# Optimization experiments

Hardware: AMD Instinct MI355X
Metric: run time of the kernel (lower is better)

## Reference

```python
import jax, jax.numpy as jnp
import numpy as np

N = 524288          # batch size
NUM_SD = 64         # socio-demographic chars
H = 128             # hidden size of TasteParams MLP
NUM_ALT_FEAT = 9    # alternative features
NUM_CLASSES = 3
# utility_structure: class k -> (start, end) column slice of x
SEGMENTS = [(0, 3), (3, 6), (6, 9)]


def setup_inputs() -> dict:
    key = jax.random.key(0)
    ks = jax.random.split(key, 8)
    s = 0.05
    return {
        "x": jax.random.normal(ks[0], (N, NUM_ALT_FEAT), jnp.float32),
        "z": jax.random.normal(ks[1], (N, NUM_SD), jnp.float32),
        "W1": jax.random.normal(ks[2], (NUM_SD, H), jnp.float32) * s,
        "b1": jax.random.normal(ks[3], (H,), jnp.float32) * s,
        "W2": jax.random.normal(ks[4], (H, H), jnp.float32) * s,
        "b2": jax.random.normal(ks[5], (H,), jnp.float32) * s,
        "W3": jax.random.normal(ks[6], (H, NUM_ALT_FEAT + NUM_CLASSES), jnp.float32) * s,
        "b3": jax.random.normal(ks[7], (NUM_ALT_FEAT + NUM_CLASSES,), jnp.float32) * s,
    }


def _forward(x, z, W1, b1, W2, b2, W3, b3):
    # TasteParams MLP: Linear-ReLU-Linear-ReLU-Linear
    h = jax.nn.relu(z @ W1 + b1)
    h = jax.nn.relu(h @ W2 + b2)
    b = h @ W3 + b3                        # (N, 12)
    # monotonic_constraints (num_classes==3, func_intercept=True)
    b = jnp.concatenate([
        -jax.nn.relu(-b[:, :6]),
        b[:, 6:7],
        -jax.nn.relu(-b[:, 7:9]),
        b[:, -NUM_CLASSES:],
    ], axis=1)
    taste = b[:, :NUM_ALT_FEAT]            # (N, 9)
    intercept = b[:, -NUM_CLASSES:]        # (N, 3)
    # MNL_layer with b: per-segment elementwise mult + reduce into logits column
    prod = x * taste                       # (N, 9)
    logits = jnp.stack(
        [prod[:, lo:hi].sum(axis=1) for (lo, hi) in SEGMENTS], axis=1
    )                                      # (N, 3)
    return logits + intercept


def reference(x, z, W1, b1, W2, b2, W3, b3):
    return _forward(x, z, W1, b1, W2, b2, W3, b3)
```

## Files before the change

### kernel.cpp

```cpp
#include <hip/hip_runtime.h>
#include <hip/hip_bf16.h>


typedef __bf16 bf16x8 __attribute__((ext_vector_type(8)));
typedef float  f32x16 __attribute__((ext_vector_type(16)));
typedef unsigned int uint2v __attribute__((ext_vector_type(2)));
typedef unsigned int uint4v __attribute__((ext_vector_type(4)));

#define MFMA32(a, b, c) __builtin_amdgcn_mfma_f32_32x32x16_bf16((a), (b), (c), 0, 0, 0)
#define PIN_AGPR(v) asm("" : "+a"(v))

#define SW3 0
#define SW1 1536
#define SW2 9728
#define SB1 26112
#define SB2 26240
#define SB3 26368
#define SMEM_ELTS 26384

#define NBLK    512
#define NTILE   16384
#define WSTRIDE (NBLK * 4)

__device__ __forceinline__ unsigned pkbf(float lo, float hi) {
  unsigned short lb = __builtin_bit_cast(unsigned short, (__bf16)lo);
  unsigned short hb = __builtin_bit_cast(unsigned short, (__bf16)hi);
  return ((unsigned)hb << 16) | (unsigned)lb;
}

template <int SUB>
__device__ __forceinline__ bf16x8 mk_bfrag(const f32x16 h) {
  constexpr int B = SUB * 8;
  unsigned p01 = pkbf(h[B + 0], h[B + 1]);
  unsigned p23 = pkbf(h[B + 2], h[B + 3]);
  unsigned p45 = pkbf(h[B + 4], h[B + 5]);
  unsigned p67 = pkbf(h[B + 6], h[B + 7]);
  unsigned d0, d1, d2, d3;
#if __has_builtin(__builtin_amdgcn_permlane32_swap)
  uint2v r1 = __builtin_amdgcn_permlane32_swap(p01, p45, false, false);
  uint2v r2 = __builtin_amdgcn_permlane32_swap(p23, p67, false, false);
  d0 = r1[0]; d2 = r1[1];
  d1 = r2[0]; d3 = r2[1];
#else
  int hi = (threadIdx.x >> 5) & 1;
  unsigned sp01 = (unsigned)__shfl_xor((int)p01, 32, 64);
  unsigned sp23 = (unsigned)__shfl_xor((int)p23, 32, 64);
  unsigned sp45 = (unsigned)__shfl_xor((int)p45, 32, 64);
  unsigned sp67 = (unsigned)__shfl_xor((int)p67, 32, 64);
  d0 = hi ? sp45 : p01;
  d2 = hi ? p45  : sp01;
  d1 = hi ? sp67 : p23;
  d3 = hi ? p67  : sp23;
#endif
  uint4v t; t[0] = d0; t[1] = d1; t[2] = d2; t[3] = d3;
  return __builtin_bit_cast(bf16x8, t);
}

__device__ __forceinline__ bf16x8 ldw(const __bf16* sm, int vaddr, int imm) {
  return *(const bf16x8*)((const char*)sm + vaddr + imm);
}

__device__ __forceinline__ bf16x8 biasA(__bf16 v) {
  bf16x8 f;
  #pragma unroll
  for (int i = 0; i < 8; ++i) f[i] = (__bf16)0.0f;
  f[0] = v;
  return f;
}

__global__ __launch_bounds__(256, 2)
void tastenet_kernel(const float* __restrict__ x, const float* __restrict__ z,
                     const float* __restrict__ W1, const float* __restrict__ b1,
                     const float* __restrict__ W2, const float* __restrict__ b2,
                     const float* __restrict__ W3, const float* __restrict__ b3,
                     float* __restrict__ out) {
  __shared__ __align__(16) __bf16 sm[SMEM_ELTS];
  const int tid = threadIdx.x;
  unsigned* smw = (unsigned*)sm;

  for (int i = tid; i < 4096; i += 256) {
    int m = i & 127, k = (i >> 7) * 2;
    smw[SW1 / 2 + m * 32 + (((k >> 3) ^ (m & 7)) << 2) + ((k >> 1) & 3)] =
        pkbf(W1[k * 128 + m], W1[(k + 1) * 128 + m]);
  }
  for (int i = tid; i < 8192; i += 256) {
    int m = i & 127, k = (i >> 7) * 2;
    smw[SW2 / 2 + m * 64 + (((k >> 3) ^ (m & 7)) << 2) + ((k >> 1) & 3)] =
        pkbf(W2[k * 128 + m], W2[(k + 1) * 128 + m]);
  }
  for (int i = tid; i < 768; i += 256) {
    int kk = i / 12, m = i - kk * 12, k = kk * 2;
    smw[SW3 / 2 + m * 64 + (((k >> 3) ^ (m & 7)) << 2) + ((k >> 1) & 3)] =
        pkbf(W3[k * 12 + m], W3[(k + 1) * 12 + m]);
  }
  if (tid < 128) { sm[SB1 + tid] = (__bf16)b1[tid]; sm[SB2 + tid] = (__bf16)b2[tid]; }
  if (tid < 12)  sm[SB3 + tid] = (__bf16)b3[tid];
  __syncthreads();

  const int wave = tid >> 6;
  const int lane = tid & 63;
  const int q    = lane >> 5;
  const int n    = lane & 31;
  const int s8   = n & 7;
  const int eq   = q ^ (s8 & 1);
  const int sh   = s8 >> 1;

  int aw1[4], aw2[4];
  #pragma unroll
  for (int j = 0; j < 4; ++j) {
    aw1[j] = n * 128 + eq * 16 + 32 * (j ^ sh);
    aw2[j] = n * 256 + eq * 16 + 32 * (j ^ sh);
  }

  bf16x8 ones;
  #pragma unroll
  for (int i = 0; i < 8; ++i) ones[i] = (__bf16)0.0f;
  if (q == 0) ones[0] = (__bf16)1.0f;
  PIN_AGPR(ones);

  bf16x8 ba1[4], ba2[4], ba3;
  #pragma unroll
  for (int f = 0; f < 4; ++f) {
    ba1[f] = biasA((q == 0) ? sm[SB1 + f * 32 + n] : (__bf16)0.0f);
    ba2[f] = biasA((q == 0) ? sm[SB2 + f * 32 + n] : (__bf16)0.0f);
    PIN_AGPR(ba1[f]); PIN_AGPR(ba2[f]);
  }
  ba3 = biasA((q == 0 && n < 12) ? sm[SB3 + n] : (__bf16)0.0f);
  PIN_AGPR(ba3);

  f32x16 zeroC;
  #pragma unroll
  for (int i = 0; i < 16; ++i) zeroC[i] = 0.0f;
  PIN_AGPR(zeroC);

  const int wid = blockIdx.x * 4 + wave;

  float4 zv[8];
  {
    const float* zr = z + ((long)wid * 32 + n) * 64;
    #pragma unroll
    for (int kt = 0; kt < 4; ++kt) {
      zv[2 * kt]     = *(const float4*)(zr + kt * 16 + q * 8);
      zv[2 * kt + 1] = *(const float4*)(zr + kt * 16 + q * 8 + 4);
    }
  }

  #pragma unroll 1
  for (int t = wid; t < NTILE; t += WSTRIDE) {
    const long row = (long)t * 32 + n;

    const float* xr = x + row * 9;
    float xv0 = xr[q * 4 + 0], xv1 = xr[q * 4 + 1];
    float xv2 = xr[q * 4 + 2], xv3 = xr[q * 4 + 3];
    float xv4 = xr[8];

    bf16x8 bz[4];
    #pragma unroll
    for (int kt = 0; kt < 4; ++kt) {
      float4 a = zv[2 * kt], b = zv[2 * kt + 1];
      bf16x8 f;
      f[0] = (__bf16)a.x; f[1] = (__bf16)a.y; f[2] = (__bf16)a.z; f[3] = (__bf16)a.w;
      f[4] = (__bf16)b.x; f[5] = (__bf16)b.y; f[6] = (__bf16)b.z; f[7] = (__bf16)b.w;
      bz[kt] = f;
    }

    if (t + WSTRIDE < NTILE) {
      const float* zr = z + ((long)(t + WSTRIDE) * 32 + n) * 64;
      #pragma unroll
      for (int kt = 0; kt < 4; ++kt) {
        zv[2 * kt]     = *(const float4*)(zr + kt * 16 + q * 8);
        zv[2 * kt + 1] = *(const float4*)(zr + kt * 16 + q * 8 + 4);
      }
    }

    bf16x8 bf2[8];
    #pragma unroll
    for (int fp = 0; fp < 2; ++fp) {
      f32x16 aA = MFMA32(ba1[2 * fp + 0], ones, zeroC);
      f32x16 aB = MFMA32(ba1[2 * fp + 1], ones, zeroC);
      PIN_AGPR(aA); PIN_AGPR(aB);
      #pragma unroll
      for (int kt = 0; kt < 4; ++kt) {
        aA = MFMA32(ldw(sm, aw1[kt], SW1 * 2 + (2 * fp + 0) * 4096), bz[kt], aA);
        aB = MFMA32(ldw(sm, aw1[kt], SW1 * 2 + (2 * fp + 1) * 4096), bz[kt], aB);
      }
      #pragma unroll
      for (int i = 0; i < 16; ++i) { aA[i] = fmaxf(aA[i], 0.0f); aB[i] = fmaxf(aB[i], 0.0f); }
      bf2[4 * fp + 0] = mk_bfrag<0>(aA);
      bf2[4 * fp + 1] = mk_bfrag<1>(aA);
      bf2[4 * fp + 2] = mk_bfrag<0>(aB);
      bf2[4 * fp + 3] = mk_bfrag<1>(aB);
    }

    f32x16 acc3 = MFMA32(ba3, ones, zeroC);
    PIN_AGPR(acc3);
    #pragma unroll
    for (int fp = 0; fp < 2; ++fp) {
      f32x16 aA = MFMA32(ba2[2 * fp + 0], ones, zeroC);
      f32x16 aB = MFMA32(ba2[2 * fp + 1], ones, zeroC);
      PIN_AGPR(aA); PIN_AGPR(aB);
      #pragma unroll
      for (int kt = 0; kt < 8; ++kt) {
        aA = MFMA32(ldw(sm, aw2[kt & 3], SW2 * 2 + (2 * fp + 0) * 8192 + 128 * (kt >> 2)),
                    bf2[kt], aA);
        aB = MFMA32(ldw(sm, aw2[kt & 3], SW2 * 2 + (2 * fp + 1) * 8192 + 128 * (kt >> 2)),
                    bf2[kt], aB);
      }
      #pragma unroll
      for (int i = 0; i < 16; ++i) { aA[i] = fmaxf(aA[i], 0.0f); aB[i] = fmaxf(aB[i], 0.0f); }
      acc3 = MFMA32(ldw(sm, aw2[0], SW3 * 2 + 128 * fp), mk_bfrag<0>(aA), acc3);
      acc3 = MFMA32(ldw(sm, aw2[1], SW3 * 2 + 128 * fp), mk_bfrag<1>(aA), acc3);
      acc3 = MFMA32(ldw(sm, aw2[2], SW3 * 2 + 128 * fp), mk_bfrag<0>(aB), acc3);
      acc3 = MFMA32(ldw(sm, aw2[3], SW3 * 2 + 128 * fp), mk_bfrag<1>(aB), acc3);
    }

    float t0 = acc3[0], t1 = acc3[1], t2 = acc3[2], t3 = acc3[3];
    float t4 = acc3[4], t5 = acc3[5], t6 = acc3[6], t7 = acc3[7];
    float o0 = 0.f, o1 = 0.f, o2 = 0.f, g1v = 0.f, g2v = 0.f;
    if (q == 0) {
      t0 = fminf(t0, 0.0f); t1 = fminf(t1, 0.0f);
      t2 = fminf(t2, 0.0f); t3 = fminf(t3, 0.0f);
      t4 = fminf(t4, 0.0f);
      o0 = xv0 * t0 + xv1 * t1 + xv2 * t2 + t5;
      o1 = xv3 * t3 + t6;
      o2 = xv4 * t4 + t7;
    } else {
      t0 = fminf(t0, 0.0f); t1 = fminf(t1, 0.0f);
      t3 = fminf(t3, 0.0f);
      g1v = xv0 * t0 + xv1 * t1;
      g2v = xv2 * t2 + xv3 * t3;
    }
    float a1v = __shfl_xor(g1v, 32, 64);
    float a2v = __shfl_xor(g2v, 32, 64);
    if (q == 0) {
      float* op = out + row * 3;
      op[0] = o0;
      op[1] = o1 + a1v;
      op[2] = o2 + a2v;
    }
  }
}

extern "C" void kernel_launch(void* const* d_in, const int* in_sizes, int n_in,
                              void* d_out, int out_size, void* d_ws, size_t ws_size,
                              hipStream_t stream) {
  const float* x  = (const float*)d_in[0];
  const float* z  = (const float*)d_in[1];
  const float* W1 = (const float*)d_in[2];
  const float* b1 = (const float*)d_in[3];
  const float* W2 = (const float*)d_in[4];
  const float* b2 = (const float*)d_in[5];
  const float* W3 = (const float*)d_in[6];
  const float* b3 = (const float*)d_in[7];
  tastenet_kernel<<<dim3(NBLK), dim3(256), 0, stream>>>(
      x, z, W1, b1, W2, b2, W3, b3, (float*)d_out);
}
```

Before: 234.7 us.

## Reload bias fragments from LDS per tile and raise occupancy to three blocks

Stops keeping the nine bias A-fragments pinned in AGPRs for the whole kernel. Each tile now reloads them from LDS, using an opaque zero offset so the compiler cannot hoist the loads back out of the loop. The z-to-bf16 conversion for the next tile moves to the middle of the current tile, behind a sched_barrier. The freed registers let launch_bounds ask for 3 blocks per CU, and the grid grows to 768 blocks to match; the cost is extra LDS reads and VALU work on every tile.

After: 281.9 us. +20.1%, slower.

```diff
diff --git a/kernel.cpp b/kernel.cpp
--- a/kernel.cpp
+++ b/kernel.cpp
@@ -18,7 +18,7 @@
 #define SB3 26368
 #define SMEM_ELTS 26384
 
-#define NBLK    512
+#define NBLK    768
 #define NTILE   16384
 #define WSTRIDE (NBLK * 4)
 
@@ -68,7 +68,7 @@
   return f;
 }
 
-__global__ __launch_bounds__(256, 2)
+__global__ __launch_bounds__(256, 3)
 void tastenet_kernel(const float* __restrict__ x, const float* __restrict__ z,
                      const float* __restrict__ W1, const float* __restrict__ b1,
                      const float* __restrict__ W2, const float* __restrict__ b2,
@@ -118,16 +118,6 @@
   if (q == 0) ones[0] = (__bf16)1.0f;
   PIN_AGPR(ones);
 
-  bf16x8 ba1[4], ba2[4], ba3;
-  #pragma unroll
-  for (int f = 0; f < 4; ++f) {
-    ba1[f] = biasA((q == 0) ? sm[SB1 + f * 32 + n] : (__bf16)0.0f);
-    ba2[f] = biasA((q == 0) ? sm[SB2 + f * 32 + n] : (__bf16)0.0f);
-    PIN_AGPR(ba1[f]); PIN_AGPR(ba2[f]);
-  }
-  ba3 = biasA((q == 0 && n < 12) ? sm[SB3 + n] : (__bf16)0.0f);
-  PIN_AGPR(ba3);
-
   f32x16 zeroC;
   #pragma unroll
   for (int i = 0; i < 16; ++i) zeroC[i] = 0.0f;
@@ -136,6 +126,7 @@
   const int wid = blockIdx.x * 4 + wave;
 
   float4 zv[8];
+  bf16x8 bz[4];
   {
     const float* zr = z + ((long)wid * 32 + n) * 64;
     #pragma unroll
@@ -143,18 +134,6 @@
       zv[2 * kt]     = *(const float4*)(zr + kt * 16 + q * 8);
       zv[2 * kt + 1] = *(const float4*)(zr + kt * 16 + q * 8 + 4);
     }
-  }
-
-  #pragma unroll 1
-  for (int t = wid; t < NTILE; t += WSTRIDE) {
-    const long row = (long)t * 32 + n;
-
-    const float* xr = x + row * 9;
-    float xv0 = xr[q * 4 + 0], xv1 = xr[q * 4 + 1];
-    float xv2 = xr[q * 4 + 2], xv3 = xr[q * 4 + 3];
-    float xv4 = xr[8];
-
-    bf16x8 bz[4];
     #pragma unroll
     for (int kt = 0; kt < 4; ++kt) {
       float4 a = zv[2 * kt], b = zv[2 * kt + 1];
@@ -163,6 +142,19 @@
       f[4] = (__bf16)b.x; f[5] = (__bf16)b.y; f[6] = (__bf16)b.z; f[7] = (__bf16)b.w;
       bz[kt] = f;
     }
+  }
+
+  #pragma unroll 1
+  for (int t = wid; t < NTILE; t += WSTRIDE) {
+    const long row = (long)t * 32 + n;
+
+    int zt;
+    asm volatile("v_mov_b32 %0, 0" : "=v"(zt));
+
+    const float* xr = x + row * 9;
+    float xv0 = xr[q * 4 + 0], xv1 = xr[q * 4 + 1];
+    float xv2 = xr[q * 4 + 2], xv3 = xr[q * 4 + 3];
+    float xv4 = xr[8];
 
     if (t + WSTRIDE < NTILE) {
       const float* zr = z + ((long)(t + WSTRIDE) * 32 + n) * 64;
@@ -176,8 +168,12 @@
     bf16x8 bf2[8];
     #pragma unroll
     for (int fp = 0; fp < 2; ++fp) {
-      f32x16 aA = MFMA32(ba1[2 * fp + 0], ones, zeroC);
-      f32x16 aB = MFMA32(ba1[2 * fp + 1], ones, zeroC);
+      f32x16 aA = MFMA32(
+          biasA((q == 0) ? sm[SB1 + zt + (2 * fp + 0) * 32 + n] : (__bf16)0.0f),
+          ones, zeroC);
+      f32x16 aB = MFMA32(
+          biasA((q == 0) ? sm[SB1 + zt + (2 * fp + 1) * 32 + n] : (__bf16)0.0f),
+          ones, zeroC);
       PIN_AGPR(aA); PIN_AGPR(aB);
       #pragma unroll
       for (int kt = 0; kt < 4; ++kt) {
@@ -192,12 +188,29 @@
       bf2[4 * fp + 3] = mk_bfrag<1>(aB);
     }
 
-    f32x16 acc3 = MFMA32(ba3, ones, zeroC);
+    if (t + WSTRIDE < NTILE) {
+      #pragma unroll
+      for (int kt = 0; kt < 4; ++kt) {
+        float4 a = zv[2 * kt], b = zv[2 * kt + 1];
+        bf16x8 f;
+        f[0] = (__bf16)a.x; f[1] = (__bf16)a.y; f[2] = (__bf16)a.z; f[3] = (__bf16)a.w;
+        f[4] = (__bf16)b.x; f[5] = (__bf16)b.y; f[6] = (__bf16)b.z; f[7] = (__bf16)b.w;
+        bz[kt] = f;
+      }
+    }
+    __builtin_amdgcn_sched_barrier(0);
+
+    f32x16 acc3 = MFMA32(
+        biasA((q == 0 && n < 12) ? sm[SB3 + zt + n] : (__bf16)0.0f), ones, zeroC);
     PIN_AGPR(acc3);
     #pragma unroll
     for (int fp = 0; fp < 2; ++fp) {
-      f32x16 aA = MFMA32(ba2[2 * fp + 0], ones, zeroC);
-      f32x16 aB = MFMA32(ba2[2 * fp + 1], ones, zeroC);
+      f32x16 aA = MFMA32(
+          biasA((q == 0) ? sm[SB2 + zt + (2 * fp + 0) * 32 + n] : (__bf16)0.0f),
+          ones, zeroC);
+      f32x16 aB = MFMA32(
+          biasA((q == 0) ? sm[SB2 + zt + (2 * fp + 1) * 32 + n] : (__bf16)0.0f),
+          ones, zeroC);
       PIN_AGPR(aA); PIN_AGPR(aB);
       #pragma unroll
       for (int kt = 0; kt < 8; ++kt) {
```

## Widen MFMA chains to four accumulators and split layer-3 reduction

Applied to the files above, without the earlier changes.

Layers 1 and 2 now keep four independent 32x32 accumulators live at once instead of processing two at a time, which gives the MFMA pipeline more independent work and hides dependency latency. The bf16 conversion of the next tile's z is moved into the loop body after layer 1, behind a scheduling barrier. The layer-3 reduction is split into two accumulator chains that are summed at the end to shorten the serial dependency. In exchange, more AGPR/VGPR pressure could hurt the occupancy of two blocks per CU or cause spills.

Measured after the change: 247.6 us. 1.06x slower.

```diff
diff --git a/kernel.cpp b/kernel.cpp
--- a/kernel.cpp
+++ b/kernel.cpp
@@ -136,6 +136,7 @@
   const int wid = blockIdx.x * 4 + wave;
 
   float4 zv[8];
+  bf16x8 bz[4];
   {
     const float* zr = z + ((long)wid * 32 + n) * 64;
     #pragma unroll
@@ -143,18 +144,6 @@
       zv[2 * kt]     = *(const float4*)(zr + kt * 16 + q * 8);
       zv[2 * kt + 1] = *(const float4*)(zr + kt * 16 + q * 8 + 4);
     }
-  }
-
-  #pragma unroll 1
-  for (int t = wid; t < NTILE; t += WSTRIDE) {
-    const long row = (long)t * 32 + n;
-
-    const float* xr = x + row * 9;
-    float xv0 = xr[q * 4 + 0], xv1 = xr[q * 4 + 1];
-    float xv2 = xr[q * 4 + 2], xv3 = xr[q * 4 + 3];
-    float xv4 = xr[8];
-
-    bf16x8 bz[4];
     #pragma unroll
     for (int kt = 0; kt < 4; ++kt) {
       float4 a = zv[2 * kt], b = zv[2 * kt + 1];
@@ -163,6 +152,16 @@
       f[4] = (__bf16)b.x; f[5] = (__bf16)b.y; f[6] = (__bf16)b.z; f[7] = (__bf16)b.w;
       bz[kt] = f;
     }
+  }
+
+  #pragma unroll 1
+  for (int t = wid; t < NTILE; t += WSTRIDE) {
+    const long row = (long)t * 32 + n;
+
+    const float* xr = x + row * 9;
+    float xv0 = xr[q * 4 + 0], xv1 = xr[q * 4 + 1];
+    float xv2 = xr[q * 4 + 2], xv3 = xr[q * 4 + 3];
+    float xv4 = xr[8];
 
     if (t + WSTRIDE < NTILE) {
       const float* zr = z + ((long)(t + WSTRIDE) * 32 + n) * 64;
@@ -173,49 +172,76 @@
       }
     }
 
+    f32x16 d0 = MFMA32(ba1[0], ones, zeroC);
+    f32x16 d1 = MFMA32(ba1[1], ones, zeroC);
+    f32x16 d2 = MFMA32(ba1[2], ones, zeroC);
+    f32x16 d3 = MFMA32(ba1[3], ones, zeroC);
+    PIN_AGPR(d0); PIN_AGPR(d1); PIN_AGPR(d2); PIN_AGPR(d3);
+    #pragma unroll
+    for (int kt = 0; kt < 4; ++kt) {
+      d0 = MFMA32(ldw(sm, aw1[kt], SW1 * 2 + 0 * 4096), bz[kt], d0);
+      d1 = MFMA32(ldw(sm, aw1[kt], SW1 * 2 + 1 * 4096), bz[kt], d1);
+      d2 = MFMA32(ldw(sm, aw1[kt], SW1 * 2 + 2 * 4096), bz[kt], d2);
+      d3 = MFMA32(ldw(sm, aw1[kt], SW1 * 2 + 3 * 4096), bz[kt], d3);
+    }
+    #pragma unroll
+    for (int i = 0; i < 16; ++i) {
+      d0[i] = fmaxf(d0[i], 0.0f); d1[i] = fmaxf(d1[i], 0.0f);
+      d2[i] = fmaxf(d2[i], 0.0f); d3[i] = fmaxf(d3[i], 0.0f);
+    }
     bf16x8 bf2[8];
-    #pragma unroll
-    for (int fp = 0; fp < 2; ++fp) {
-      f32x16 aA = MFMA32(ba1[2 * fp + 0], ones, zeroC);
-      f32x16 aB = MFMA32(ba1[2 * fp + 1], ones, zeroC);
-      PIN_AGPR(aA); PIN_AGPR(aB);
+    bf2[0] = mk_bfrag<0>(d0); bf2[1] = mk_bfrag<1>(d0);
+    bf2[2] = mk_bfrag<0>(d1); bf2[3] = mk_bfrag<1>(d1);
+    bf2[4] = mk_bfrag<0>(d2); bf2[5] = mk_bfrag<1>(d2);
+    bf2[6] = mk_bfrag<0>(d3); bf2[7] = mk_bfrag<1>(d3);
+
+    if (t + WSTRIDE < NTILE) {
       #pragma unroll
       for (int kt = 0; kt < 4; ++kt) {
-        aA = MFMA32(ldw(sm, aw1[kt], SW1 * 2 + (2 * fp + 0) * 4096), bz[kt], aA);
-        aB = MFMA32(ldw(sm, aw1[kt], SW1 * 2 + (2 * fp + 1) * 4096), bz[kt], aB);
+        float4 a = zv[2 * kt], b = zv[2 * kt + 1];
+        bf16x8 f;
+        f[0] = (__bf16)a.x; f[1] = (__bf16)a.y; f[2] = (__bf16)a.z; f[3] = (__bf16)a.w;
+        f[4] = (__bf16)b.x; f[5] = (__bf16)b.y; f[6] = (__bf16)b.z; f[7] = (__bf16)b.w;
+        bz[kt] = f;
       }
-      #pragma unroll
-      for (int i = 0; i < 16; ++i) { aA[i] = fmaxf(aA[i], 0.0f); aB[i] = fmaxf(aB[i], 0.0f); }
-      bf2[4 * fp + 0] = mk_bfrag<0>(aA);
-      bf2[4 * fp + 1] = mk_bfrag<1>(aA);
-      bf2[4 * fp + 2] = mk_bfrag<0>(aB);
-      bf2[4 * fp + 3] = mk_bfrag<1>(aB);
-    }
-
-    f32x16 acc3 = MFMA32(ba3, ones, zeroC);
-    PIN_AGPR(acc3);
-    #pragma unroll
-    for (int fp = 0; fp < 2; ++fp) {
-      f32x16 aA = MFMA32(ba2[2 * fp + 0], ones, zeroC);
-      f32x16 aB = MFMA32(ba2[2 * fp + 1], ones, zeroC);
-      PIN_AGPR(aA); PIN_AGPR(aB);
-      #pragma unroll
-      for (int kt = 0; kt < 8; ++kt) {
-        aA = MFMA32(ldw(sm, aw2[kt & 3], SW2 * 2 + (2 * fp + 0) * 8192 + 128 * (kt >> 2)),
-                    bf2[kt], aA);
-        aB = MFMA32(ldw(sm, aw2[kt & 3], SW2 * 2 + (2 * fp + 1) * 8192 + 128 * (kt >> 2)),
-                    bf2[kt], aB);
-      }
-      #pragma unroll
-      for (int i = 0; i < 16; ++i) { aA[i] = fmaxf(aA[i], 0.0f); aB[i] = fmaxf(aB[i], 0.0f); }
-      acc3 = MFMA32(ldw(sm, aw2[0], SW3 * 2 + 128 * fp), mk_bfrag<0>(aA), acc3);
-      acc3 = MFMA32(ldw(sm, aw2[1], SW3 * 2 + 128 * fp), mk_bfrag<1>(aA), acc3);
-      acc3 = MFMA32(ldw(sm, aw2[2], SW3 * 2 + 128 * fp), mk_bfrag<0>(aB), acc3);
-      acc3 = MFMA32(ldw(sm, aw2[3], SW3 * 2 + 128 * fp), mk_bfrag<1>(aB), acc3);
-    }
-
-    float t0 = acc3[0], t1 = acc3[1], t2 = acc3[2], t3 = acc3[3];
-    float t4 = acc3[4], t5 = acc3[5], t6 = acc3[6], t7 = acc3[7];
+    }
+    __builtin_amdgcn_sched_barrier(0);
+
+    f32x16 c0 = MFMA32(ba2[0], ones, zeroC);
+    f32x16 c1 = MFMA32(ba2[1], ones, zeroC);
+    f32x16 c2 = MFMA32(ba2[2], ones, zeroC);
+    f32x16 c3 = MFMA32(ba2[3], ones, zeroC);
+    PIN_AGPR(c0); PIN_AGPR(c1); PIN_AGPR(c2); PIN_AGPR(c3);
+    #pragma unroll
+    for (int kt = 0; kt < 8; ++kt) {
+      const int ro = 128 * (kt >> 2);
+      c0 = MFMA32(ldw(sm, aw2[kt & 3], SW2 * 2 + 0 * 8192 + ro), bf2[kt], c0);
+      c1 = MFMA32(ldw(sm, aw2[kt & 3], SW2 * 2 + 1 * 8192 + ro), bf2[kt], c1);
+      c2 = MFMA32(ldw(sm, aw2[kt & 3], SW2 * 2 + 2 * 8192 + ro), bf2[kt], c2);
+      c3 = MFMA32(ldw(sm, aw2[kt & 3], SW2 * 2 + 3 * 8192 + ro), bf2[kt], c3);
+    }
+    #pragma unroll
+    for (int i = 0; i < 16; ++i) {
+      c0[i] = fmaxf(c0[i], 0.0f); c1[i] = fmaxf(c1[i], 0.0f);
+      c2[i] = fmaxf(c2[i], 0.0f); c3[i] = fmaxf(c3[i], 0.0f);
+    }
+
+    f32x16 a3a = MFMA32(ba3, ones, zeroC);
+    PIN_AGPR(a3a);
+    a3a = MFMA32(ldw(sm, aw2[0], SW3 * 2 + 0),   mk_bfrag<0>(c0), a3a);
+    f32x16 a3b = MFMA32(ldw(sm, aw2[0], SW3 * 2 + 128), mk_bfrag<0>(c2), zeroC);
+    PIN_AGPR(a3b);
+    a3a = MFMA32(ldw(sm, aw2[1], SW3 * 2 + 0),   mk_bfrag<1>(c0), a3a);
+    a3b = MFMA32(ldw(sm, aw2[1], SW3 * 2 + 128), mk_bfrag<1>(c2), a3b);
+    a3a = MFMA32(ldw(sm, aw2[2], SW3 * 2 + 0),   mk_bfrag<0>(c1), a3a);
+    a3b = MFMA32(ldw(sm, aw2[2], SW3 * 2 + 128), mk_bfrag<0>(c3), a3b);
+    a3a = MFMA32(ldw(sm, aw2[3], SW3 * 2 + 0),   mk_bfrag<1>(c1), a3a);
+    a3b = MFMA32(ldw(sm, aw2[3], SW3 * 2 + 128), mk_bfrag<1>(c3), a3b);
+
+    float t0 = a3a[0] + a3b[0], t1 = a3a[1] + a3b[1];
+    float t2 = a3a[2] + a3b[2], t3 = a3a[3] + a3b[3];
+    float t4 = a3a[4] + a3b[4], t5 = a3a[5] + a3b[5];
+    float t6 = a3a[6] + a3b[6], t7 = a3a[7] + a3b[7];
     float o0 = 0.f, o1 = 0.f, o2 = 0.f, g1v = 0.f, g2v = 0.f;
     if (q == 0) {
       t0 = fminf(t0, 0.0f); t1 = fminf(t1, 0.0f);
```

## Prefetch z tiles directly into swizzled LDS with global_load_lds

Applied to the files above, without the earlier changes.

Replaces the register-held float4 prefetch of the next z tile with asynchronous global-to-LDS DMA loads into a per-wave, XOR-swizzled LDS slot. Each tile's z fragments are then read back from LDS and converted to bf16. The block grows to 8 waves (512 threads) over 256 blocks, and LDS use rises accordingly. The goal is to free the registers that held in-flight z data and to keep global loads asynchronous. The cost is more LDS traffic, a full vmcnt wait at every iteration, and the large LDS footprint limiting residency to one block per CU.

Measured after the change: 241.1 us. 1.03x slower.

```diff
diff --git a/kernel.cpp b/kernel.cpp
--- a/kernel.cpp
+++ b/kernel.cpp
@@ -16,11 +16,20 @@
 #define SB1 26112
 #define SB2 26240
 #define SB3 26368
-#define SMEM_ELTS 26384
-
-#define NBLK    512
+#define ZS_BYTE 52768
+#define SMEM_ELTS (26384 + 32768)
+
+#define NBLK    256
+#define NTHR    512
 #define NTILE   16384
-#define WSTRIDE (NBLK * 4)
+#define WSTRIDE (NBLK * 8)
+
+typedef __attribute__((address_space(3))) unsigned int lds_u32;
+typedef __attribute__((address_space(1))) const unsigned int glb_u32;
+
+__device__ __forceinline__ void gll16(const float* g, const void* l) {
+  __builtin_amdgcn_global_load_lds((glb_u32*)g, (lds_u32*)l, 16, 0, 0);
+}
 
 __device__ __forceinline__ unsigned pkbf(float lo, float hi) {
   unsigned short lb = __builtin_bit_cast(unsigned short, (__bf16)lo);
@@ -60,6 +69,10 @@
   return *(const bf16x8*)((const char*)sm + vaddr + imm);
 }
 
+__device__ __forceinline__ float4 ldz(const __bf16* sm, int vaddr) {
+  return *(const float4*)((const char*)sm + vaddr);
+}
+
 __device__ __forceinline__ bf16x8 biasA(__bf16 v) {
   bf16x8 f;
   #pragma unroll
@@ -68,7 +81,7 @@
   return f;
 }
 
-__global__ __launch_bounds__(256, 2)
+__global__ __launch_bounds__(512, 2)
 void tastenet_kernel(const float* __restrict__ x, const float* __restrict__ z,
                      const float* __restrict__ W1, const float* __restrict__ b1,
                      const float* __restrict__ W2, const float* __restrict__ b2,
@@ -78,17 +91,17 @@
   const int tid = threadIdx.x;
   unsigned* smw = (unsigned*)sm;
 
-  for (int i = tid; i < 4096; i += 256) {
+  for (int i = tid; i < 4096; i += NTHR) {
     int m = i & 127, k = (i >> 7) * 2;
     smw[SW1 / 2 + m * 32 + (((k >> 3) ^ (m & 7)) << 2) + ((k >> 1) & 3)] =
         pkbf(W1[k * 128 + m], W1[(k + 1) * 128 + m]);
   }
-  for (int i = tid; i < 8192; i += 256) {
+  for (int i = tid; i < 8192; i += NTHR) {
     int m = i & 127, k = (i >> 7) * 2;
     smw[SW2 / 2 + m * 64 + (((k >> 3) ^ (m & 7)) << 2) + ((k >> 1) & 3)] =
         pkbf(W2[k * 128 + m], W2[(k + 1) * 128 + m]);
   }
-  for (int i = tid; i < 768; i += 256) {
+  for (int i = tid; i < 768; i += NTHR) {
     int kk = i / 12, m = i - kk * 12, k = kk * 2;
     smw[SW3 / 2 + m * 64 + (((k >> 3) ^ (m & 7)) << 2) + ((k >> 1) & 3)] =
         pkbf(W3[k * 12 + m], W3[(k + 1) * 12 + m]);
@@ -112,6 +125,22 @@
     aw2[j] = n * 256 + eq * 16 + 32 * (j ^ sh);
   }
 
+  const char* slotp = (const char*)sm + ZS_BYTE + wave * 8192;
+  const int lr = lane >> 4, lc = lane & 15;
+  int gofs[8];
+  #pragma unroll
+  for (int i = 0; i < 8; ++i) {
+    int r = 4 * i + lr;
+    gofs[i] = r * 64 + ((lc ^ (r & 15)) << 2);
+  }
+  int zrd[8];
+  #pragma unroll
+  for (int kt = 0; kt < 4; ++kt)
+    #pragma unroll
+    for (int s = 0; s < 2; ++s)
+      zrd[2 * kt + s] =
+          ZS_BYTE + wave * 8192 + n * 256 + (((4 * kt + 2 * q + s) ^ (n & 15)) << 4);
+
   bf16x8 ones;
   #pragma unroll
   for (int i = 0; i < 8; ++i) ones[i] = (__bf16)0.0f;
@@ -133,21 +162,19 @@
   for (int i = 0; i < 16; ++i) zeroC[i] = 0.0f;
   PIN_AGPR(zeroC);
 
-  const int wid = blockIdx.x * 4 + wave;
-
-  float4 zv[8];
+  const int wid = blockIdx.x * 8 + wave;
+
   {
-    const float* zr = z + ((long)wid * 32 + n) * 64;
-    #pragma unroll
-    for (int kt = 0; kt < 4; ++kt) {
-      zv[2 * kt]     = *(const float4*)(zr + kt * 16 + q * 8);
-      zv[2 * kt + 1] = *(const float4*)(zr + kt * 16 + q * 8 + 4);
-    }
+    const float* zb = z + (long)wid * 2048;
+    #pragma unroll
+    for (int i = 0; i < 8; ++i) gll16(zb + gofs[i], slotp + (i << 10));
   }
 
   #pragma unroll 1
   for (int t = wid; t < NTILE; t += WSTRIDE) {
     const long row = (long)t * 32 + n;
+
+    asm volatile("s_waitcnt vmcnt(0)" ::: "memory");
 
     const float* xr = x + row * 9;
     float xv0 = xr[q * 4 + 0], xv1 = xr[q * 4 + 1];
@@ -157,21 +184,21 @@
     bf16x8 bz[4];
     #pragma unroll
     for (int kt = 0; kt < 4; ++kt) {
-      float4 a = zv[2 * kt], b = zv[2 * kt + 1];
+      float4 a = ldz(sm, zrd[2 * kt]);
+      float4 b = ldz(sm, zrd[2 * kt + 1]);
       bf16x8 f;
       f[0] = (__bf16)a.x; f[1] = (__bf16)a.y; f[2] = (__bf16)a.z; f[3] = (__bf16)a.w;
       f[4] = (__bf16)b.x; f[5] = (__bf16)b.y; f[6] = (__bf16)b.z; f[7] = (__bf16)b.w;
       bz[kt] = f;
     }
+    __builtin_amdgcn_sched_barrier(0);
 
     if (t + WSTRIDE < NTILE) {
-      const float* zr = z + ((long)(t + WSTRIDE) * 32 + n) * 64;
-      #pragma unroll
-      for (int kt = 0; kt < 4; ++kt) {
-        zv[2 * kt]     = *(const float4*)(zr + kt * 16 + q * 8);
-        zv[2 * kt + 1] = *(const float4*)(zr + kt * 16 + q * 8 + 4);
-      }
-    }
+      const float* zb = z + (long)(t + WSTRIDE) * 2048;
+      #pragma unroll
+      for (int i = 0; i < 8; ++i) gll16(zb + gofs[i], slotp + (i << 10));
+    }
+    __builtin_amdgcn_sched_barrier(0);
 
     bf16x8 bf2[8];
     #pragma unroll
@@ -252,6 +279,6 @@
   const float* b2 = (const float*)d_in[5];
   const float* W3 = (const float*)d_in[6];
   const float* b3 = (const float*)d_in[7];
-  tastenet_kernel<<<dim3(NBLK), dim3(256), 0, stream>>>(
+  tastenet_kernel<<<dim3(NBLK), dim3(NTHR), 0, stream>>>(
       x, z, W1, b1, W2, b2, W3, b3, (float*)d_out);
 }
```
